# Performance work log

Measured on AMD Instinct MI355X. Metric: run time of the kernel, lower is better.

## Reference

```python
import jax, jax.numpy as jnp
import numpy as np
import math

B, S, D, H = 2, 2048, 1024, 16
DH = D // H

def setup_inputs() -> dict:
    key = jax.random.key(0)
    k = jax.random.split(key, 6)
    scale = 1.0 / math.sqrt(D)
    x = jax.random.normal(k[0], (B, S, D), jnp.float32)
    mask = jnp.ones((B, S), jnp.int32)
    # torch.nn.Linear weights: [out_features, in_features]
    W_q = jax.random.normal(k[1], (D, D), jnp.float32) * scale
    b_q = jnp.zeros((D,), jnp.float32)
    W_v = jax.random.normal(k[2], (D, D), jnp.float32) * scale
    W_out = jax.random.normal(k[3], (D, D), jnp.float32) * scale
    b_out = jnp.zeros((D,), jnp.float32)
    return {"x": x, "W_q": W_q, "b_q": b_q, "W_v": W_v, "W_out": W_out, "b_out": b_out, "mask": mask}

def reference(x, W_q, b_q, W_v, W_out, b_out, mask):
    inv_sqrt_dh = 1.0 / math.sqrt(DH)
    # q: [B, H, S, DH]
    q = (x @ W_q.T + b_q).reshape(B, S, H, DH).transpose(0, 2, 1, 3)
    # L2-distance attention logits: -(||q_s||^2 - 2 q_s.q_t + ||q_t||^2)/sqrt(dh)
    sq = jnp.sum(q * q, axis=-1)  # [B, H, S]
    qk = jnp.einsum('bhsd,bhtd->bhst', q, q)  # [B, H, S, S]
    logits = -(sq[..., :, None] - 2.0 * qk + sq[..., None, :]) * inv_sqrt_dh
    logits = jnp.where(mask[:, None, None, :] == 0, jnp.float32(-9e15), logits)
    w = jax.nn.softmax(logits, axis=-1)  # [B, H, S, S]
    # W_q_T[h, j, i] = W_q[i, h*DH + j] -> [H, DH, D]
    W_q_T = W_q.reshape(D, H, DH).transpose(1, 2, 0)
    # v[h, i, j] = W_v[i, h*DH + j] -> [H, D, DH]
    v = W_v.reshape(D, H, DH).transpose(1, 0, 2)
    attn = jnp.einsum('bhst,bhtd->bhsd', w, q)          # [B, H, S, DH]
    attn = jnp.einsum('bhsd,hde->bhse', attn, W_q_T)    # [B, H, S, D]
    attn = jnp.einsum('bhse,hef->bhsf', attn, v) * inv_sqrt_dh  # [B, H, S, DH]
    attn = attn.transpose(0, 2, 1, 3).reshape(B, S, D)
    return x + attn @ W_out.T + b_out
```

## Files before the change

kernel.cpp:

```cpp
#include <hip/hip_runtime.h>

#define S_LEN 2048
#define D_DIM 1024
#define NH    16
#define DHEAD 64

typedef float f32x4 __attribute__((ext_vector_type(4)));
typedef __bf16 bf16x8 __attribute__((ext_vector_type(8)));
typedef unsigned short u16;
typedef unsigned int u32;
typedef unsigned short u16x8 __attribute__((ext_vector_type(8)));
typedef unsigned short u16x4 __attribute__((ext_vector_type(4)));

__device__ __forceinline__ u16 f2bf(float f) {
    union { float f; unsigned u; } c; c.f = f;
    unsigned u = c.u + 0x7fffu + ((c.u >> 16) & 1u);
    return (u16)(u >> 16);
}

#if __has_builtin(__builtin_amdgcn_exp2f)
#define EXP2(x) __builtin_amdgcn_exp2f(x)
#else
#define EXP2(x) exp2f(x)
#endif

#define C_QK  0.36067376022224085f
#define C_SQ  0.18033688011112043f

#define MFMA16(a, b, c) __builtin_amdgcn_mfma_f32_16x16x32_bf16((a), (b), (c), 0, 0, 0)

__device__ __forceinline__ u32 pack_bf(float lo, float hi) {
    union { float f; u32 u; } a, b; a.f = lo; b.f = hi;
    return (b.u & 0xFFFF0000u) | (a.u >> 16);
}

__global__ __launch_bounds__(512, 4) void k_mega1(
    const float* __restrict__ x, const float* __restrict__ Wq,
    const float* __restrict__ Wv, const float* __restrict__ bq,
    const int* __restrict__ mask, u16* __restrict__ Qbf, u16* __restrict__ QT,
    float* __restrict__ sq05, float* __restrict__ Mpart) {
    __shared__ __align__(16) char smem[38912];
    const int tid = threadIdx.x;

    if (blockIdx.x >= 256) {
        const int id = blockIdx.x - 256;
        const int z = id & 7, h = id >> 3;
        float* Qp = (float*)smem;
        float* Vp = (float*)(smem + 16384);
        const int r = tid >> 3, seg = tid & 7;
        const int j0 = (tid >> 4) * 2;
        const int f0 = (tid & 15) * 4;
        f32x4 acc0 = {0.f, 0.f, 0.f, 0.f}, acc1 = acc0;
        for (int c = 0; c < 2; ++c) {
            const int e0 = z * 128 + c * 64;
            __syncthreads();
            const float* q = Wq + (size_t)(e0 + r) * D_DIM + h * DHEAD + seg * 8;
            const float* v = Wv + (size_t)(e0 + r) * D_DIM + h * DHEAD + seg * 8;
            *(f32x4*)&Qp[r * 64 + seg * 8]     = *(const f32x4*)q;
            *(f32x4*)&Qp[r * 64 + seg * 8 + 4] = *(const f32x4*)(q + 4);
            *(f32x4*)&Vp[r * 64 + seg * 8]     = *(const f32x4*)v;
            *(f32x4*)&Vp[r * 64 + seg * 8 + 4] = *(const f32x4*)(v + 4);
            __syncthreads();
#pragma unroll 8
            for (int e = 0; e < 64; ++e) {
                float q0 = Qp[e * 64 + j0], q1 = Qp[e * 64 + j0 + 1];
                f32x4 vv = *(const f32x4*)&Vp[e * 64 + f0];
                acc0 += q0 * vv;
                acc1 += q1 * vv;
            }
        }
        float* dst = Mpart + (size_t)z * 65536 + ((size_t)(h * 64 + j0)) * 64 + f0;
        *(f32x4*)dst        = acc0 * 0.125f;
        *(f32x4*)(dst + 64) = acc1 * 0.125f;
        return;
    }

    u16* Al = (u16*)smem;
    u16* Bl = (u16*)(smem + 18432);
    float* sqp = (float*)(smem + 36864);

    const int lane = tid & 63, w = tid >> 6;
    const int wm = w & 1, wn = w >> 1;
    const int col16 = lane & 15, quad = lane >> 4;
    const int bm = blockIdx.x & 31, bn = blockIdx.x >> 5;

    f32x4 acc[4][2];
    const f32x4 z4 = {0.f, 0.f, 0.f, 0.f};
#pragma unroll
    for (int i = 0; i < 4; ++i)
#pragma unroll
        for (int j = 0; j < 2; ++j) acc[i][j] = z4;

    const int ar = tid >> 2, as = tid & 3;
    const float* pa = x + (size_t)(bm * 128 + ar) * D_DIM + as * 16;
    const float* pb = Wq + (size_t)(bn * 128 + ar) * D_DIM + as * 16;

    f32x4 fa[4], fb[4];
#pragma unroll
    for (int i = 0; i < 4; ++i) {
        fa[i] = *(const f32x4*)(pa + i * 4);
        fb[i] = *(const f32x4*)(pb + i * 4);
    }

    for (int k0 = 0; k0 < D_DIM; k0 += 64) {
        u16x8 wa[2], wb[2];
#pragma unroll
        for (int i = 0; i < 2; ++i)
#pragma unroll
            for (int e = 0; e < 4; ++e) {
                wa[i][e] = f2bf(fa[2 * i][e]); wa[i][e + 4] = f2bf(fa[2 * i + 1][e]);
                wb[i][e] = f2bf(fb[2 * i][e]); wb[i][e + 4] = f2bf(fb[2 * i + 1][e]);
            }
        __syncthreads();
#pragma unroll
        for (int i = 0; i < 2; ++i) *(u16x8*)&Al[ar * 72 + as * 16 + i * 8] = wa[i];
#pragma unroll
        for (int i = 0; i < 2; ++i) *(u16x8*)&Bl[ar * 72 + as * 16 + i * 8] = wb[i];
        __syncthreads();
        if (k0 + 64 < D_DIM) {
#pragma unroll
            for (int i = 0; i < 4; ++i) {
                fa[i] = *(const f32x4*)(pa + k0 + 64 + i * 4);
                fb[i] = *(const f32x4*)(pb + k0 + 64 + i * 4);
            }
        }
#pragma unroll
        for (int kh = 0; kh < 2; ++kh) {
            bf16x8 af[4];
#pragma unroll
            for (int mt = 0; mt < 4; ++mt)
                af[mt] = *(const bf16x8*)&Al[(wm * 64 + mt * 16 + col16) * 72 + kh * 32 + quad * 8];
#pragma unroll
            for (int nt = 0; nt < 2; ++nt) {
                bf16x8 bfr = *(const bf16x8*)&Bl[(wn * 32 + nt * 16 + col16) * 72 + kh * 32 + quad * 8];
#pragma unroll
                for (int mt = 0; mt < 4; ++mt)
                    acc[mt][nt] = MFMA16(af[mt], bfr, acc[mt][nt]);
            }
        }
    }

    const int hh = wn >> 1;
    f32x4 ssum[4];
#pragma unroll
    for (int mt = 0; mt < 4; ++mt) ssum[mt] = z4;

    u16 qv16[2][4][4];
#pragma unroll
    for (int nt = 0; nt < 2; ++nt) {
        int col = bn * 128 + wn * 32 + nt * 16 + col16;
        float bqv = bq[col];
#pragma unroll
        for (int mt = 0; mt < 4; ++mt) {
            int row0 = bm * 128 + wm * 64 + mt * 16 + quad * 4;
#pragma unroll
            for (int rr = 0; rr < 4; ++rr) {
                float qv = acc[mt][nt][rr] + bqv;
                ssum[mt][rr] += qv * qv;
                u16 bv = f2bf(qv);
                qv16[nt][mt][rr] = bv;
                Qbf[(size_t)(row0 + rr) * D_DIM + col] = bv;
            }
        }
    }
    float vred[4][4];
#pragma unroll
    for (int mt = 0; mt < 4; ++mt)
#pragma unroll
        for (int rr = 0; rr < 4; ++rr) {
            float v = ssum[mt][rr];
            v += __shfl_xor(v, 1); v += __shfl_xor(v, 2);
            v += __shfl_xor(v, 4); v += __shfl_xor(v, 8);
            vred[mt][rr] = v;
        }
    if (col16 == 0) {
#pragma unroll
        for (int mt = 0; mt < 4; ++mt)
#pragma unroll
            for (int rr = 0; rr < 4; ++rr)
                sqp[wn * 128 + wm * 64 + mt * 16 + quad * 4 + rr] = vred[mt][rr];
    }
    __syncthreads();

    u16* Td = (u16*)smem;
#pragma unroll
    for (int nt = 0; nt < 2; ++nt) {
        int dloc = (wn & 1) * 32 + nt * 16 + col16;
#pragma unroll
        for (int mt = 0; mt < 4; ++mt) {
            int sl = wm * 64 + mt * 16 + quad * 4;
#pragma unroll
            for (int rr = 0; rr < 4; ++rr)
                Td[(hh * 64 + dloc) * 130 + sl + rr] = qv16[nt][mt][rr];
        }
    }
    __syncthreads();

    const int bb = (bm * 128) >> 11, s0 = (bm * 128) & 2047;
    if (tid < 256) {
        int r = tid & 127, hh2 = tid >> 7;
        float v = sqp[(2 * hh2) * 128 + r] + sqp[(2 * hh2 + 1) * 128 + r];
        int sidx = s0 + r;
        float o = mask[bb * S_LEN + sidx] ? v * C_SQ : 1e30f;
        sq05[((size_t)(bb * NH + bn * 2 + hh2)) * S_LEN + sidx] = o;
    }
    {
        int dr = tid >> 2, ch = tid & 3;
        int hh3 = dr >> 6, d = dr & 63;
        u16* dst = QT + ((size_t)(bb * NH + bn * 2 + hh3) * DHEAD + d) * S_LEN + s0 + ch * 32;
        const u16* src = Td + (hh3 * 64 + d) * 130 + ch * 32;
#pragma unroll
        for (int i = 0; i < 4; ++i)
            *(u16x8*)(dst + i * 8) = *(const u16x8*)(src + i * 8);
    }
}

__global__ __launch_bounds__(256, 2) void k_mega2(
    const u16* __restrict__ Qbf, const u16* __restrict__ QT,
    const float* __restrict__ sq05, u16* __restrict__ attnO,
    const float* __restrict__ Mpart, const float* __restrict__ Wout,
    u16* __restrict__ W2) {
    __shared__ __align__(16) char smem[34816];
    const int tid = threadIdx.x;

    if (blockIdx.x >= 512) {
        const int id = blockIdx.x - 512;
        const int ob = id & 15, h = id >> 4;
        float* Ms = (float*)smem;
        float* Ws = (float*)(smem + 16640);
        {
            int rr = tid >> 2, seg = tid & 3;
            const size_t mo = ((size_t)(h * 64 + rr)) * 64 + seg * 16;
            const float* ws = Wout + (size_t)(ob * 64 + rr) * D_DIM + h * DHEAD + seg * 16;
#pragma unroll
            for (int e = 0; e < 16; ++e) {
                float s = 0.f;
#pragma unroll
                for (int k = 0; k < 8; ++k) s += Mpart[mo + e + (size_t)k * 65536];
                Ms[rr * 65 + seg * 16 + e] = s;
                Ws[rr * 65 + seg * 16 + e] = ws[e];
            }
        }
        __syncthreads();
        int j = tid & 63, o0 = (tid >> 6) * 16;
        for (int oo = o0; oo < o0 + 16; ++oo) {
            float acc = 0.f;
#pragma unroll
            for (int f = 0; f < 64; ++f) acc += Ms[j * 65 + f] * Ws[oo * 65 + f];
            W2[(size_t)(ob * 64 + oo) * D_DIM + h * DHEAD + j] = f2bf(acc);
        }
        return;
    }

    u16* Kt  = (u16*)smem;
    u16* KtT = (u16*)(smem + 16384);
    float* sql = (float*)(smem + 32768);

    const int lane = tid & 63, w = tid >> 6;
    const int col16 = lane & 15, quad = lane >> 4;
    const int wq = w & 1, wk = w >> 1;
    const int bh = blockIdx.x & 31;
    const int qt = blockIdx.x >> 5;
    const int h = bh & 15;
    const int b = bh >> 4;
    const u16* qbase = Qbf + (size_t)b * S_LEN * D_DIM + h * DHEAD;
    const u16* qtbase = QT + ((size_t)(b * NH + h)) * DHEAD * S_LEN;
    const float* sqb = sq05 + ((size_t)(b * NH + h)) * S_LEN;

    bf16x8 qb[4][2];
#pragma unroll
    for (int nq = 0; nq < 4; ++nq)
#pragma unroll
        for (int k0 = 0; k0 < 2; ++k0)
            qb[nq][k0] = *(const bf16x8*)(qbase +
                (size_t)(qt * 128 + wq * 64 + nq * 16 + col16) * D_DIM + k0 * 32 + quad * 8);

    const int r00 = wk * 64 + (col16 >> 2) * 8 + (col16 & 3);
    const int swzA = (col16 & 3) | (((col16 >> 2) & 1) << 2);
    const int krow00 = r00 * 64 + (quad ^ swzA) * 8;
    const int sq00 = wk * 64 + quad * 8;
    int vrow[4];
#pragma unroll
    for (int dblk = 0; dblk < 4; ++dblk) {
        int rT = dblk * 16 + col16;
        vrow[dblk] = rT * 128 + ((wk * 8 + quad) ^ (rT & 7)) * 8;
    }

    const int kr = tid >> 1, ks = tid & 1;
    const int td = tid >> 2, ts = tid & 3;
    const int kswz = (kr & 3) | (((kr >> 3) & 1) << 2);
    const int tswz = td & 7;
    const u16* ksrc = qbase + (size_t)kr * D_DIM + ks * 32;
    const u16* tsrc = qtbase + (size_t)td * S_LEN + ts * 32;

    u16x8 pk[4], pt[4];
    float sv = 0.f;
#pragma unroll
    for (int i = 0; i < 4; ++i) pk[i] = *(const u16x8*)(ksrc + i * 8);
#pragma unroll
    for (int i = 0; i < 4; ++i) pt[i] = *(const u16x8*)(tsrc + i * 8);
    if (tid < 128) sv = sqb[tid];

    f32x4 Oacc[4][4], lacc[4];
    const f32x4 z4 = {0.f, 0.f, 0.f, 0.f};
#pragma unroll
    for (int n = 0; n < 4; ++n) {
        lacc[n] = z4;
#pragma unroll
        for (int d = 0; d < 4; ++d) Oacc[d][n] = z4;
    }
    bf16x8 ones;
    {
        union { u16x8 u; bf16x8 b; } cv;
#pragma unroll
        for (int e = 0; e < 8; ++e) cv.u[e] = 0x3F80;
        ones = cv.b;
    }

    for (int j = 0; j < S_LEN / 128; ++j) {
        __syncthreads();
#pragma unroll
        for (int i = 0; i < 4; ++i)
            *(u16x8*)(Kt + kr * 64 + ((ks * 4 + i) ^ kswz) * 8) = pk[i];
#pragma unroll
        for (int i = 0; i < 4; ++i)
            *(u16x8*)(KtT + td * 128 + ((ts * 4 + i) ^ tswz) * 8) = pt[i];
        if (tid < 128) sql[tid] = sv;
        __syncthreads();

        int jn = (j + 1) & 15;
        {
            const u16* kn = ksrc + (size_t)jn * 128 * D_DIM;
            const u16* tn = tsrc + (size_t)jn * 128;
#pragma unroll
            for (int i = 0; i < 4; ++i) pk[i] = *(const u16x8*)(kn + i * 8);
#pragma unroll
            for (int i = 0; i < 4; ++i) pt[i] = *(const u16x8*)(tn + i * 8);
            if (tid < 128) sv = sqb[jn * 128 + tid];
        }

        for (int kt = 0; kt < 2; ++kt) {
            f32x4 sacc[2][4];
#pragma unroll
            for (int kbh = 0; kbh < 2; ++kbh)
#pragma unroll
                for (int nq = 0; nq < 4; ++nq) sacc[kbh][nq] = z4;
            __builtin_amdgcn_s_setprio(1);
#pragma unroll
            for (int kbh = 0; kbh < 2; ++kbh) {
                int kro = krow00 + kt * 2048 + kbh * 256;
                bf16x8 a0 = *(const bf16x8*)(Kt + kro);
                bf16x8 a1 = *(const bf16x8*)(Kt + (kro ^ 32));
#pragma unroll
                for (int nq = 0; nq < 4; ++nq) {
                    sacc[kbh][nq] = MFMA16(a0, qb[nq][0], sacc[kbh][nq]);
                    sacc[kbh][nq] = MFMA16(a1, qb[nq][1], sacc[kbh][nq]);
                }
            }
            __builtin_amdgcn_s_setprio(0);

            bf16x8 va[4];
#pragma unroll
            for (int dblk = 0; dblk < 4; ++dblk)
                va[dblk] = *(const bf16x8*)(KtT + (vrow[dblk] ^ (kt * 32)));

            u32 pf[4][4];
#pragma unroll
            for (int kbh = 0; kbh < 2; ++kbh) {
                f32x4 sqv = *(const f32x4*)(sql + sq00 + kt * 32 + kbh * 4);
#pragma unroll
                for (int nq = 0; nq < 4; ++nq) {
                    float p0 = EXP2(fmaf(sacc[kbh][nq][0], C_QK, -sqv[0]));
                    float p1 = EXP2(fmaf(sacc[kbh][nq][1], C_QK, -sqv[1]));
                    float p2 = EXP2(fmaf(sacc[kbh][nq][2], C_QK, -sqv[2]));
                    float p3 = EXP2(fmaf(sacc[kbh][nq][3], C_QK, -sqv[3]));
                    pf[nq][kbh * 2]     = pack_bf(p0, p1);
                    pf[nq][kbh * 2 + 1] = pack_bf(p2, p3);
                }
            }

            __builtin_amdgcn_s_setprio(1);
#pragma unroll
            for (int nq = 0; nq < 4; ++nq) {
                union { u32 u[4]; bf16x8 b; } pb;
#pragma unroll
                for (int i = 0; i < 4; ++i) pb.u[i] = pf[nq][i];
                lacc[nq] = MFMA16(ones, pb.b, lacc[nq]);
#pragma unroll
                for (int dblk = 0; dblk < 4; ++dblk)
                    Oacc[dblk][nq] = MFMA16(va[dblk], pb.b, Oacc[dblk][nq]);
            }
            __builtin_amdgcn_s_setprio(0);
        }
    }

    __syncthreads();
    float* Obuf = (float*)smem;
    float* lred = (float*)(smem + 32768);
    if (wk == 1) {
#pragma unroll
        for (int dblk = 0; dblk < 4; ++dblk)
#pragma unroll
            for (int nq = 0; nq < 4; ++nq)
                *(f32x4*)(Obuf + ((wq * 16 + dblk * 4 + nq) * 64 + lane) * 4) = Oacc[dblk][nq];
#pragma unroll
        for (int nq = 0; nq < 4; ++nq)
            lred[(wq * 4 + nq) * 64 + lane] = lacc[nq][0];
    }
    __syncthreads();
    if (wk == 0) {
        float rinv[4];
#pragma unroll
        for (int nq = 0; nq < 4; ++nq)
            rinv[nq] = 1.f / (lacc[nq][0] + lred[(wq * 4 + nq) * 64 + lane]);
        u16* obase = attnO + (size_t)b * S_LEN * D_DIM + h * DHEAD;
#pragma unroll
        for (int dblk = 0; dblk < 4; ++dblk)
#pragma unroll
            for (int nq = 0; nq < 4; ++nq) {
                f32x4 o = Oacc[dblk][nq] + *(const f32x4*)(Obuf + ((wq * 16 + dblk * 4 + nq) * 64 + lane) * 4);
                int q = qt * 128 + wq * 64 + nq * 16 + col16;
                u16x4 pkk;
#pragma unroll
                for (int rr = 0; rr < 4; ++rr) pkk[rr] = f2bf(o[rr] * rinv[nq]);
                *(u16x4*)(obase + (size_t)q * D_DIM + dblk * 16 + quad * 4) = pkk;
            }
    }
}

__global__ __launch_bounds__(256, 4) void k_oproj(
    const u16* __restrict__ attnO, const u16* __restrict__ W2,
    const float* __restrict__ x, const float* __restrict__ bout, float* __restrict__ out) {
    __shared__ __align__(16) char smem[27648];
    u16* Al = (u16*)smem;
    u16* Bl = (u16*)(smem + 9216);
    const int tid = threadIdx.x, lane = tid & 63, wn = tid >> 6;
    const int col16 = lane & 15, quad = lane >> 4;
    const int bm = blockIdx.x, bn = blockIdx.y;

    f32x4 acc[4][2];
    const f32x4 z4 = {0.f, 0.f, 0.f, 0.f};
#pragma unroll
    for (int i = 0; i < 4; ++i)
#pragma unroll
        for (int j = 0; j < 2; ++j) acc[i][j] = z4;

    const int arA = tid >> 2, asA = tid & 3;
    const int brB = tid >> 1, bsB = tid & 1;
    const u16* pa = attnO + (size_t)(bm * 64 + arA) * D_DIM + asA * 16;
    const u16* pb = W2 + (size_t)(bn * 128 + brB) * D_DIM + bsB * 32;

    u16x8 ra[2], rb[4];
#pragma unroll
    for (int i = 0; i < 2; ++i) ra[i] = *(const u16x8*)(pa + i * 8);
#pragma unroll
    for (int i = 0; i < 4; ++i) rb[i] = *(const u16x8*)(pb + i * 8);

    for (int k0 = 0; k0 < D_DIM; k0 += 64) {
        __syncthreads();
#pragma unroll
        for (int i = 0; i < 2; ++i) *(u16x8*)&Al[arA * 72 + asA * 16 + i * 8] = ra[i];
#pragma unroll
        for (int i = 0; i < 4; ++i) *(u16x8*)&Bl[brB * 72 + bsB * 32 + i * 8] = rb[i];
        __syncthreads();
        if (k0 + 64 < D_DIM) {
#pragma unroll
            for (int i = 0; i < 2; ++i) ra[i] = *(const u16x8*)(pa + k0 + 64 + i * 8);
#pragma unroll
            for (int i = 0; i < 4; ++i) rb[i] = *(const u16x8*)(pb + k0 + 64 + i * 8);
        }
#pragma unroll
        for (int kh = 0; kh < 2; ++kh) {
            bf16x8 af[4];
#pragma unroll
            for (int mt = 0; mt < 4; ++mt)
                af[mt] = *(const bf16x8*)&Al[(mt * 16 + col16) * 72 + kh * 32 + quad * 8];
#pragma unroll
            for (int nt = 0; nt < 2; ++nt) {
                bf16x8 bfr = *(const bf16x8*)&Bl[(wn * 32 + nt * 16 + col16) * 72 + kh * 32 + quad * 8];
#pragma unroll
                for (int mt = 0; mt < 4; ++mt)
                    acc[mt][nt] = MFMA16(af[mt], bfr, acc[mt][nt]);
            }
        }
    }
#pragma unroll
    for (int nt = 0; nt < 2; ++nt) {
        int col = bn * 128 + wn * 32 + nt * 16 + col16;
        float bv = bout[col];
#pragma unroll
        for (int mt = 0; mt < 4; ++mt) {
            int row0 = bm * 64 + mt * 16 + quad * 4;
#pragma unroll
            for (int rr = 0; rr < 4; ++rr) {
                size_t idx = (size_t)(row0 + rr) * D_DIM + col;
                out[idx] = acc[mt][nt][rr] + x[idx] + bv;
            }
        }
    }
}

extern "C" void kernel_launch(void* const* d_in, const int* in_sizes, int n_in,
                              void* d_out, int out_size, void* d_ws, size_t ws_size,
                              hipStream_t stream) {
    const float* x    = (const float*)d_in[0];
    const float* Wq   = (const float*)d_in[1];
    const float* bq   = (const float*)d_in[2];
    const float* Wv   = (const float*)d_in[3];
    const float* Wout = (const float*)d_in[4];
    const float* bout = (const float*)d_in[5];
    const int*   mask = (const int*)d_in[6];
    float* out = (float*)d_out;

    char* ws = (char*)d_ws;
    u16*   Qbf   = (u16*)(ws);
    u16*   QT    = (u16*)(ws + (8u << 20));
    u16*   attnO = (u16*)(ws + (16u << 20));
    u16*   W2    = (u16*)(ws + (24u << 20));
    float* Mpart = (float*)(ws + (26u << 20));
    float* sq05  = (float*)(ws + (28u << 20));

    k_mega1<<<dim3(384), dim3(512), 0, stream>>>(x, Wq, Wv, bq, mask, Qbf, QT, sq05, Mpart);
    k_mega2<<<dim3(768), dim3(256), 0, stream>>>(Qbf, QT, sq05, attnO, Mpart, Wout, W2);
    k_oproj<<<dim3(64, 8), dim3(256), 0, stream>>>(attnO, W2, x, bout, out);
}
```

Before: 187.3 us.

## Load K/V fragments directly from global memory instead of staging through LDS

Removes the shared-memory staging of K, K-transpose and squared-norm tiles, along with the two block barriers per iteration and the register prefetch. Each wave now reads its MFMA operand fragments straight from global memory (relying on L2/L1 hits) and the s_setprio hints are dropped. This removes LDS write/read traffic and synchronisation, but exposes global load latency with no explicit prefetch and makes each wave issue redundant global reads.

Result: slower. 215.6 us (+15.1%).

```diff
diff --git a/kernel.cpp b/kernel.cpp
--- a/kernel.cpp
+++ b/kernel.cpp
@@ -252,10 +252,6 @@
         return;
     }
 
-    u16* Kt  = (u16*)smem;
-    u16* KtT = (u16*)(smem + 16384);
-    float* sql = (float*)(smem + 32768);
-
     const int lane = tid & 63, w = tid >> 6;
     const int col16 = lane & 15, quad = lane >> 4;
     const int wq = w & 1, wk = w >> 1;
@@ -275,31 +271,10 @@
             qb[nq][k0] = *(const bf16x8*)(qbase +
                 (size_t)(qt * 128 + wq * 64 + nq * 16 + col16) * D_DIM + k0 * 32 + quad * 8);
 
-    const int r00 = wk * 64 + (col16 >> 2) * 8 + (col16 & 3);
-    const int swzA = (col16 & 3) | (((col16 >> 2) & 1) << 2);
-    const int krow00 = r00 * 64 + (quad ^ swzA) * 8;
-    const int sq00 = wk * 64 + quad * 8;
-    int vrow[4];
-#pragma unroll
-    for (int dblk = 0; dblk < 4; ++dblk) {
-        int rT = dblk * 16 + col16;
-        vrow[dblk] = rT * 128 + ((wk * 8 + quad) ^ (rT & 7)) * 8;
-    }
-
-    const int kr = tid >> 1, ks = tid & 1;
-    const int td = tid >> 2, ts = tid & 3;
-    const int kswz = (kr & 3) | (((kr >> 3) & 1) << 2);
-    const int tswz = td & 7;
-    const u16* ksrc = qbase + (size_t)kr * D_DIM + ks * 32;
-    const u16* tsrc = qtbase + (size_t)td * S_LEN + ts * 32;
-
-    u16x8 pk[4], pt[4];
-    float sv = 0.f;
-#pragma unroll
-    for (int i = 0; i < 4; ++i) pk[i] = *(const u16x8*)(ksrc + i * 8);
-#pragma unroll
-    for (int i = 0; i < 4; ++i) pt[i] = *(const u16x8*)(tsrc + i * 8);
-    if (tid < 128) sv = sqb[tid];
+    const int rowpat = (col16 >> 2) * 8 + (col16 & 3);
+    const u16* abase = qbase + (size_t)(wk * 64 + rowpat) * D_DIM + quad * 8;
+    const u16* vbase = qtbase + (size_t)col16 * S_LEN + wk * 64 + quad * 8;
+    const float* sqwb = sqb + wk * 64 + quad * 8;
 
     f32x4 Oacc[4][4], lacc[4];
     const f32x4 z4 = {0.f, 0.f, 0.f, 0.f};
@@ -318,68 +293,52 @@
     }
 
     for (int j = 0; j < S_LEN / 128; ++j) {
-        __syncthreads();
-#pragma unroll
-        for (int i = 0; i < 4; ++i)
-            *(u16x8*)(Kt + kr * 64 + ((ks * 4 + i) ^ kswz) * 8) = pk[i];
-#pragma unroll
-        for (int i = 0; i < 4; ++i)
-            *(u16x8*)(KtT + td * 128 + ((ts * 4 + i) ^ tswz) * 8) = pt[i];
-        if (tid < 128) sql[tid] = sv;
-        __syncthreads();
-
-        int jn = (j + 1) & 15;
-        {
-            const u16* kn = ksrc + (size_t)jn * 128 * D_DIM;
-            const u16* tn = tsrc + (size_t)jn * 128;
-#pragma unroll
-            for (int i = 0; i < 4; ++i) pk[i] = *(const u16x8*)(kn + i * 8);
-#pragma unroll
-            for (int i = 0; i < 4; ++i) pt[i] = *(const u16x8*)(tn + i * 8);
-            if (tid < 128) sv = sqb[jn * 128 + tid];
-        }
-
+#pragma unroll
         for (int kt = 0; kt < 2; ++kt) {
+            const int kb = j * 128 + kt * 32;
+
+            bf16x8 a[2][2];
+#pragma unroll
+            for (int kbh = 0; kbh < 2; ++kbh) {
+                const u16* ap = abase + (size_t)(kb + kbh * 4) * D_DIM;
+                a[kbh][0] = *(const bf16x8*)(ap);
+                a[kbh][1] = *(const bf16x8*)(ap + 32);
+            }
+            f32x4 sqv[2];
+            sqv[0] = *(const f32x4*)(sqwb + kb);
+            sqv[1] = *(const f32x4*)(sqwb + kb + 4);
+            bf16x8 va[4];
+#pragma unroll
+            for (int dblk = 0; dblk < 4; ++dblk)
+                va[dblk] = *(const bf16x8*)(vbase + (size_t)(dblk * 16) * S_LEN + kb);
+
             f32x4 sacc[2][4];
 #pragma unroll
             for (int kbh = 0; kbh < 2; ++kbh)
 #pragma unroll
                 for (int nq = 0; nq < 4; ++nq) sacc[kbh][nq] = z4;
-            __builtin_amdgcn_s_setprio(1);
+#pragma unroll
+            for (int kbh = 0; kbh < 2; ++kbh)
+#pragma unroll
+                for (int nq = 0; nq < 4; ++nq) {
+                    sacc[kbh][nq] = MFMA16(a[kbh][0], qb[nq][0], sacc[kbh][nq]);
+                    sacc[kbh][nq] = MFMA16(a[kbh][1], qb[nq][1], sacc[kbh][nq]);
+                }
+
+            u32 pf[4][4];
 #pragma unroll
             for (int kbh = 0; kbh < 2; ++kbh) {
-                int kro = krow00 + kt * 2048 + kbh * 256;
-                bf16x8 a0 = *(const bf16x8*)(Kt + kro);
-                bf16x8 a1 = *(const bf16x8*)(Kt + (kro ^ 32));
 #pragma unroll
                 for (int nq = 0; nq < 4; ++nq) {
-                    sacc[kbh][nq] = MFMA16(a0, qb[nq][0], sacc[kbh][nq]);
-                    sacc[kbh][nq] = MFMA16(a1, qb[nq][1], sacc[kbh][nq]);
-                }
-            }
-            __builtin_amdgcn_s_setprio(0);
-
-            bf16x8 va[4];
-#pragma unroll
-            for (int dblk = 0; dblk < 4; ++dblk)
-                va[dblk] = *(const bf16x8*)(KtT + (vrow[dblk] ^ (kt * 32)));
-
-            u32 pf[4][4];
-#pragma unroll
-            for (int kbh = 0; kbh < 2; ++kbh) {
-                f32x4 sqv = *(const f32x4*)(sql + sq00 + kt * 32 + kbh * 4);
-#pragma unroll
-                for (int nq = 0; nq < 4; ++nq) {
-                    float p0 = EXP2(fmaf(sacc[kbh][nq][0], C_QK, -sqv[0]));
-                    float p1 = EXP2(fmaf(sacc[kbh][nq][1], C_QK, -sqv[1]));
-                    float p2 = EXP2(fmaf(sacc[kbh][nq][2], C_QK, -sqv[2]));
-                    float p3 = EXP2(fmaf(sacc[kbh][nq][3], C_QK, -sqv[3]));
+                    float p0 = EXP2(fmaf(sacc[kbh][nq][0], C_QK, -sqv[kbh][0]));
+                    float p1 = EXP2(fmaf(sacc[kbh][nq][1], C_QK, -sqv[kbh][1]));
+                    float p2 = EXP2(fmaf(sacc[kbh][nq][2], C_QK, -sqv[kbh][2]));
+                    float p3 = EXP2(fmaf(sacc[kbh][nq][3], C_QK, -sqv[kbh][3]));
                     pf[nq][kbh * 2]     = pack_bf(p0, p1);
                     pf[nq][kbh * 2 + 1] = pack_bf(p2, p3);
                 }
             }
 
-            __builtin_amdgcn_s_setprio(1);
 #pragma unroll
             for (int nq = 0; nq < 4; ++nq) {
                 union { u32 u[4]; bf16x8 b; } pb;
@@ -390,7 +349,6 @@
                 for (int dblk = 0; dblk < 4; ++dblk)
                     Oacc[dblk][nq] = MFMA16(va[dblk], pb.b, Oacc[dblk][nq]);
             }
-            __builtin_amdgcn_s_setprio(0);
         }
     }
 
```

## Double-buffer K tiles in LDS, drop setprio, use packed bf16 convert

Applied to the files above, without the earlier changes.

The attention loop now keeps two LDS buffers for the K, K-transpose and squared-norm tiles. The next tile is written while the current one is consumed, which cuts the loop from two barriers per iteration to one and prefetches two tiles ahead. The setprio hints around the MFMA sections are removed. The projection GEMM's float-to-bf16 rounding is replaced with the hardware packed convert instruction. The larger LDS footprint (about 65KB per block) may reduce how many blocks fit per CU below the launch-bounds target of two.

New measurement: 185.0 us. About the same (-1.2%).

```diff
diff --git a/kernel.cpp b/kernel.cpp
--- a/kernel.cpp
+++ b/kernel.cpp
@@ -16,6 +16,12 @@
     union { float f; unsigned u; } c; c.f = f;
     unsigned u = c.u + 0x7fffu + ((c.u >> 16) & 1u);
     return (u16)(u >> 16);
+}
+
+__device__ __forceinline__ u32 cvtpk(float lo, float hi) {
+    u32 r;
+    asm("v_cvt_pk_bf16_f32 %0, %1, %2" : "=v"(r) : "v"(lo), "v"(hi));
+    return r;
 }
 
 #if __has_builtin(__builtin_amdgcn_exp2f)
@@ -103,19 +109,23 @@
     }
 
     for (int k0 = 0; k0 < D_DIM; k0 += 64) {
-        u16x8 wa[2], wb[2];
-#pragma unroll
-        for (int i = 0; i < 2; ++i)
-#pragma unroll
-            for (int e = 0; e < 4; ++e) {
-                wa[i][e] = f2bf(fa[2 * i][e]); wa[i][e + 4] = f2bf(fa[2 * i + 1][e]);
-                wb[i][e] = f2bf(fb[2 * i][e]); wb[i][e + 4] = f2bf(fb[2 * i + 1][e]);
-            }
+        union { u32 w[4]; u16x8 v; } wa[2], wb[2];
+#pragma unroll
+        for (int i = 0; i < 2; ++i) {
+            wa[i].w[0] = cvtpk(fa[2 * i][0], fa[2 * i][1]);
+            wa[i].w[1] = cvtpk(fa[2 * i][2], fa[2 * i][3]);
+            wa[i].w[2] = cvtpk(fa[2 * i + 1][0], fa[2 * i + 1][1]);
+            wa[i].w[3] = cvtpk(fa[2 * i + 1][2], fa[2 * i + 1][3]);
+            wb[i].w[0] = cvtpk(fb[2 * i][0], fb[2 * i][1]);
+            wb[i].w[1] = cvtpk(fb[2 * i][2], fb[2 * i][3]);
+            wb[i].w[2] = cvtpk(fb[2 * i + 1][0], fb[2 * i + 1][1]);
+            wb[i].w[3] = cvtpk(fb[2 * i + 1][2], fb[2 * i + 1][3]);
+        }
         __syncthreads();
 #pragma unroll
-        for (int i = 0; i < 2; ++i) *(u16x8*)&Al[ar * 72 + as * 16 + i * 8] = wa[i];
-#pragma unroll
-        for (int i = 0; i < 2; ++i) *(u16x8*)&Bl[ar * 72 + as * 16 + i * 8] = wb[i];
+        for (int i = 0; i < 2; ++i) *(u16x8*)&Al[ar * 72 + as * 16 + i * 8] = wa[i].v;
+#pragma unroll
+        for (int i = 0; i < 2; ++i) *(u16x8*)&Bl[ar * 72 + as * 16 + i * 8] = wb[i].v;
         __syncthreads();
         if (k0 + 64 < D_DIM) {
 #pragma unroll
@@ -220,7 +230,7 @@
     const float* __restrict__ sq05, u16* __restrict__ attnO,
     const float* __restrict__ Mpart, const float* __restrict__ Wout,
     u16* __restrict__ W2) {
-    __shared__ __align__(16) char smem[34816];
+    __shared__ __align__(16) char smem[66560];
     const int tid = threadIdx.x;
 
     if (blockIdx.x >= 512) {
@@ -251,10 +261,6 @@
         }
         return;
     }
-
-    u16* Kt  = (u16*)smem;
-    u16* KtT = (u16*)(smem + 16384);
-    float* sql = (float*)(smem + 32768);
 
     const int lane = tid & 63, w = tid >> 6;
     const int col16 = lane & 15, quad = lane >> 4;
@@ -317,27 +323,56 @@
         ones = cv.b;
     }
 
+    {
+        u16* KtW  = (u16*)smem;
+        u16* KtTW = (u16*)(smem + 16384);
+        float* sqlW = (float*)(smem + 65536);
+#pragma unroll
+        for (int i = 0; i < 4; ++i)
+            *(u16x8*)(KtW + kr * 64 + ((ks * 4 + i) ^ kswz) * 8) = pk[i];
+#pragma unroll
+        for (int i = 0; i < 4; ++i)
+            *(u16x8*)(KtTW + td * 128 + ((ts * 4 + i) ^ tswz) * 8) = pt[i];
+        if (tid < 128) sqlW[tid] = sv;
+    }
+    {
+        const u16* kn = ksrc + (size_t)128 * D_DIM;
+        const u16* tn = tsrc + 128;
+#pragma unroll
+        for (int i = 0; i < 4; ++i) pk[i] = *(const u16x8*)(kn + i * 8);
+#pragma unroll
+        for (int i = 0; i < 4; ++i) pt[i] = *(const u16x8*)(tn + i * 8);
+        if (tid < 128) sv = sqb[128 + tid];
+    }
+    __syncthreads();
+
     for (int j = 0; j < S_LEN / 128; ++j) {
-        __syncthreads();
-#pragma unroll
-        for (int i = 0; i < 4; ++i)
-            *(u16x8*)(Kt + kr * 64 + ((ks * 4 + i) ^ kswz) * 8) = pk[i];
-#pragma unroll
-        for (int i = 0; i < 4; ++i)
-            *(u16x8*)(KtT + td * 128 + ((ts * 4 + i) ^ tswz) * 8) = pt[i];
-        if (tid < 128) sql[tid] = sv;
-        __syncthreads();
-
-        int jn = (j + 1) & 15;
-        {
-            const u16* kn = ksrc + (size_t)jn * 128 * D_DIM;
-            const u16* tn = tsrc + (size_t)jn * 128;
+        const int cur = j & 1;
+        if (j < 15) {
+            u16* KtW  = (u16*)(smem + (cur ^ 1) * 32768);
+            u16* KtTW = (u16*)(smem + 16384 + (cur ^ 1) * 32768);
+            float* sqlW = (float*)(smem + 65536) + (cur ^ 1) * 128;
+#pragma unroll
+            for (int i = 0; i < 4; ++i)
+                *(u16x8*)(KtW + kr * 64 + ((ks * 4 + i) ^ kswz) * 8) = pk[i];
+#pragma unroll
+            for (int i = 0; i < 4; ++i)
+                *(u16x8*)(KtTW + td * 128 + ((ts * 4 + i) ^ tswz) * 8) = pt[i];
+            if (tid < 128) sqlW[tid] = sv;
+        }
+        if (j < 14) {
+            const u16* kn = ksrc + (size_t)(j + 2) * 128 * D_DIM;
+            const u16* tn = tsrc + (size_t)(j + 2) * 128;
 #pragma unroll
             for (int i = 0; i < 4; ++i) pk[i] = *(const u16x8*)(kn + i * 8);
 #pragma unroll
             for (int i = 0; i < 4; ++i) pt[i] = *(const u16x8*)(tn + i * 8);
-            if (tid < 128) sv = sqb[jn * 128 + tid];
-        }
+            if (tid < 128) sv = sqb[(j + 2) * 128 + tid];
+        }
+
+        const u16* Kt  = (const u16*)(smem + cur * 32768);
+        const u16* KtT = (const u16*)(smem + 16384 + cur * 32768);
+        const float* sql = (const float*)(smem + 65536) + cur * 128;
 
         for (int kt = 0; kt < 2; ++kt) {
             f32x4 sacc[2][4];
@@ -345,7 +380,6 @@
             for (int kbh = 0; kbh < 2; ++kbh)
 #pragma unroll
                 for (int nq = 0; nq < 4; ++nq) sacc[kbh][nq] = z4;
-            __builtin_amdgcn_s_setprio(1);
 #pragma unroll
             for (int kbh = 0; kbh < 2; ++kbh) {
                 int kro = krow00 + kt * 2048 + kbh * 256;
@@ -357,7 +391,6 @@
                     sacc[kbh][nq] = MFMA16(a1, qb[nq][1], sacc[kbh][nq]);
                 }
             }
-            __builtin_amdgcn_s_setprio(0);
 
             bf16x8 va[4];
 #pragma unroll
@@ -379,7 +412,6 @@
                 }
             }
 
-            __builtin_amdgcn_s_setprio(1);
 #pragma unroll
             for (int nq = 0; nq < 4; ++nq) {
                 union { u32 u[4]; bf16x8 b; } pb;
@@ -390,11 +422,10 @@
                 for (int dblk = 0; dblk < 4; ++dblk)
                     Oacc[dblk][nq] = MFMA16(va[dblk], pb.b, Oacc[dblk][nq]);
             }
-            __builtin_amdgcn_s_setprio(0);
-        }
-    }
-
-    __syncthreads();
+        }
+        __syncthreads();
+    }
+
     float* Obuf = (float*)smem;
     float* lred = (float*)(smem + 32768);
     if (wk == 1) {
```

## Pre-convert x and W_q to bf16 in a prep kernel; drop setprio in attention

Applied to the files above, without the earlier changes.

Adds a k_prep kernel that converts x and W_q to bf16 with the packed v_cvt_pk_bf16_f32 instruction and writes them into workspace regions that later kernels reuse. The Q-projection GEMM then loads bf16 directly, halving its global traffic and removing per-element rounding from its main loop. Separately, the s_setprio hints around the MFMA blocks in the attention kernel are removed. The trade is an extra launch plus a full read and write pass over x and W_q, and conversion now rounds to nearest-even instead of the old manual rounding.

Result: faster. 178.4 us (-4.7%).

```diff
diff --git a/kernel.cpp b/kernel.cpp
--- a/kernel.cpp
+++ b/kernel.cpp
@@ -18,6 +18,17 @@
     return (u16)(u >> 16);
 }
 
+__device__ __forceinline__ u32 cvtpk(float lo, float hi) {
+    u32 r;
+    asm("v_cvt_pk_bf16_f32 %0, %1, %2" : "=v"(r) : "v"(lo), "v"(hi));
+    return r;
+}
+
+__device__ __forceinline__ u32 pack_bf(float lo, float hi) {
+    union { float f; u32 u; } a, b; a.f = lo; b.f = hi;
+    return (b.u & 0xFFFF0000u) | (a.u >> 16);
+}
+
 #if __has_builtin(__builtin_amdgcn_exp2f)
 #define EXP2(x) __builtin_amdgcn_exp2f(x)
 #else
@@ -29,15 +40,30 @@
 
 #define MFMA16(a, b, c) __builtin_amdgcn_mfma_f32_16x16x32_bf16((a), (b), (c), 0, 0, 0)
 
-__device__ __forceinline__ u32 pack_bf(float lo, float hi) {
-    union { float f; u32 u; } a, b; a.f = lo; b.f = hi;
-    return (b.u & 0xFFFF0000u) | (a.u >> 16);
+__global__ __launch_bounds__(256) void k_prep(
+    const float* __restrict__ x, const float* __restrict__ Wq,
+    u16* __restrict__ xbf, u16* __restrict__ Wqbf) {
+    const size_t NX = (size_t)2 * S_LEN * D_DIM / 8;
+    const size_t NW = (size_t)D_DIM * D_DIM / 8;
+    for (size_t c = (size_t)blockIdx.x * 256 + threadIdx.x; c < NX + NW;
+         c += (size_t)gridDim.x * 256) {
+        const float* src; u16* dst; size_t off;
+        if (c < NX) { src = x;  dst = xbf;  off = c * 8; }
+        else        { src = Wq; dst = Wqbf; off = (c - NX) * 8; }
+        f32x4 a = *(const f32x4*)(src + off);
+        f32x4 b = *(const f32x4*)(src + off + 4);
+        union { u32 w[4]; u16x8 v; } o;
+        o.w[0] = cvtpk(a[0], a[1]); o.w[1] = cvtpk(a[2], a[3]);
+        o.w[2] = cvtpk(b[0], b[1]); o.w[3] = cvtpk(b[2], b[3]);
+        *(u16x8*)(dst + off) = o.v;
+    }
 }
 
 __global__ __launch_bounds__(512, 4) void k_mega1(
-    const float* __restrict__ x, const float* __restrict__ Wq,
-    const float* __restrict__ Wv, const float* __restrict__ bq,
-    const int* __restrict__ mask, u16* __restrict__ Qbf, u16* __restrict__ QT,
+    const u16* __restrict__ xbf, const u16* __restrict__ Wqbf,
+    const float* __restrict__ Wq, const float* __restrict__ Wv,
+    const float* __restrict__ bq, const int* __restrict__ mask,
+    u16* __restrict__ Qbf, u16* __restrict__ QT,
     float* __restrict__ sq05, float* __restrict__ Mpart) {
     __shared__ __align__(16) char smem[38912];
     const int tid = threadIdx.x;
@@ -92,37 +118,27 @@
         for (int j = 0; j < 2; ++j) acc[i][j] = z4;
 
     const int ar = tid >> 2, as = tid & 3;
-    const float* pa = x + (size_t)(bm * 128 + ar) * D_DIM + as * 16;
-    const float* pb = Wq + (size_t)(bn * 128 + ar) * D_DIM + as * 16;
-
-    f32x4 fa[4], fb[4];
-#pragma unroll
-    for (int i = 0; i < 4; ++i) {
-        fa[i] = *(const f32x4*)(pa + i * 4);
-        fb[i] = *(const f32x4*)(pb + i * 4);
-    }
+    const u16* pa = xbf + (size_t)(bm * 128 + ar) * D_DIM + as * 16;
+    const u16* pb = Wqbf + (size_t)(bn * 128 + ar) * D_DIM + as * 16;
+
+    u16x8 ra[2], rb[2];
+#pragma unroll
+    for (int i = 0; i < 2; ++i) ra[i] = *(const u16x8*)(pa + i * 8);
+#pragma unroll
+    for (int i = 0; i < 2; ++i) rb[i] = *(const u16x8*)(pb + i * 8);
 
     for (int k0 = 0; k0 < D_DIM; k0 += 64) {
-        u16x8 wa[2], wb[2];
-#pragma unroll
-        for (int i = 0; i < 2; ++i)
-#pragma unroll
-            for (int e = 0; e < 4; ++e) {
-                wa[i][e] = f2bf(fa[2 * i][e]); wa[i][e + 4] = f2bf(fa[2 * i + 1][e]);
-                wb[i][e] = f2bf(fb[2 * i][e]); wb[i][e + 4] = f2bf(fb[2 * i + 1][e]);
-            }
-        __syncthreads();
-#pragma unroll
-        for (int i = 0; i < 2; ++i) *(u16x8*)&Al[ar * 72 + as * 16 + i * 8] = wa[i];
-#pragma unroll
-        for (int i = 0; i < 2; ++i) *(u16x8*)&Bl[ar * 72 + as * 16 + i * 8] = wb[i];
+        __syncthreads();
+#pragma unroll
+        for (int i = 0; i < 2; ++i) *(u16x8*)&Al[ar * 72 + as * 16 + i * 8] = ra[i];
+#pragma unroll
+        for (int i = 0; i < 2; ++i) *(u16x8*)&Bl[ar * 72 + as * 16 + i * 8] = rb[i];
         __syncthreads();
         if (k0 + 64 < D_DIM) {
 #pragma unroll
-            for (int i = 0; i < 4; ++i) {
-                fa[i] = *(const f32x4*)(pa + k0 + 64 + i * 4);
-                fb[i] = *(const f32x4*)(pb + k0 + 64 + i * 4);
-            }
+            for (int i = 0; i < 2; ++i) ra[i] = *(const u16x8*)(pa + k0 + 64 + i * 8);
+#pragma unroll
+            for (int i = 0; i < 2; ++i) rb[i] = *(const u16x8*)(pb + k0 + 64 + i * 8);
         }
 #pragma unroll
         for (int kh = 0; kh < 2; ++kh) {
@@ -345,7 +361,6 @@
             for (int kbh = 0; kbh < 2; ++kbh)
 #pragma unroll
                 for (int nq = 0; nq < 4; ++nq) sacc[kbh][nq] = z4;
-            __builtin_amdgcn_s_setprio(1);
 #pragma unroll
             for (int kbh = 0; kbh < 2; ++kbh) {
                 int kro = krow00 + kt * 2048 + kbh * 256;
@@ -357,7 +372,6 @@
                     sacc[kbh][nq] = MFMA16(a1, qb[nq][1], sacc[kbh][nq]);
                 }
             }
-            __builtin_amdgcn_s_setprio(0);
 
             bf16x8 va[4];
 #pragma unroll
@@ -379,7 +393,6 @@
                 }
             }
 
-            __builtin_amdgcn_s_setprio(1);
 #pragma unroll
             for (int nq = 0; nq < 4; ++nq) {
                 union { u32 u[4]; bf16x8 b; } pb;
@@ -390,7 +403,6 @@
                 for (int dblk = 0; dblk < 4; ++dblk)
                     Oacc[dblk][nq] = MFMA16(va[dblk], pb.b, Oacc[dblk][nq]);
             }
-            __builtin_amdgcn_s_setprio(0);
         }
     }
 
@@ -519,8 +531,11 @@
     u16*   W2    = (u16*)(ws + (24u << 20));
     float* Mpart = (float*)(ws + (26u << 20));
     float* sq05  = (float*)(ws + (28u << 20));
-
-    k_mega1<<<dim3(384), dim3(512), 0, stream>>>(x, Wq, Wv, bq, mask, Qbf, QT, sq05, Mpart);
+    u16*   xbf   = attnO;
+    u16*   Wqbf  = W2;
+
+    k_prep<<<dim3(2048), dim3(256), 0, stream>>>(x, Wq, xbf, Wqbf);
+    k_mega1<<<dim3(384), dim3(512), 0, stream>>>(xbf, Wqbf, Wq, Wv, bq, mask, Qbf, QT, sq05, Mpart);
     k_mega2<<<dim3(768), dim3(256), 0, stream>>>(Qbf, QT, sq05, attnO, Mpart, Wout, W2);
     k_oproj<<<dim3(64, 8), dim3(256), 0, stream>>>(attnO, W2, x, bout, out);
 }
```
